# Kernel tuning notes

Measured on AMD Instinct MI355X. Metric: run time of the kernel, lower is better.

## Reference

```python
import jax, jax.numpy as jnp
import numpy as np

GENE_NUM = 3000
N_NODES = 50000
N_EDGES = 1000000
DIM = 128


def setup_inputs() -> dict:
    key = jax.random.key(0)
    ks = jax.random.split(key, 8)
    h = jax.random.normal(ks[0], (N_NODES, DIM), dtype=jnp.float32)
    alpha = jax.random.normal(ks[1], (GENE_NUM + 2,), dtype=jnp.float32)
    edge_weight = jax.random.uniform(ks[2], (N_EDGES,), dtype=jnp.float32)
    # Xavier-uniform Linear weight, zero bias
    gain = float(np.sqrt(2.0))  # calculate_gain('relu')
    bound = gain * np.sqrt(6.0 / (DIM + DIM))
    W = jax.random.uniform(ks[3], (DIM, DIM), minval=-bound, maxval=bound, dtype=jnp.float32)
    b = jnp.zeros((DIM,), dtype=jnp.float32)
    # node ids: genes 0..GENE_NUM-1 have id = gene index (>=0); cells have id = -1 (<0)
    node_id = jnp.concatenate([
        jnp.arange(GENE_NUM, dtype=jnp.int64),
        -jnp.ones((N_NODES - GENE_NUM,), dtype=jnp.int64),
    ])
    edge_src = jax.random.randint(ks[4], (N_EDGES,), 0, N_NODES, dtype=jnp.int64)
    edge_dst = jax.random.randint(ks[5], (N_EDGES,), 0, N_NODES, dtype=jnp.int64)
    return {"h": h, "alpha": alpha, "edge_weight": edge_weight, "W": W, "b": b,
            "node_id": node_id, "edge_src": edge_src, "edge_dst": edge_dst}


def reference(h, alpha, edge_weight, W, b, node_id, edge_src, edge_dst):
    gene_num = alpha.shape[0] - 2
    src_id = node_id[edge_src]  # [E]
    dst_id = node_id[edge_dst]  # [E]
    # default: cell self-loop alpha -> index gene_num + 1
    idx = jnp.full(edge_src.shape, gene_num + 1, dtype=jnp.int32)
    idx = jnp.where((src_id >= 0) & (dst_id < 0), src_id.astype(jnp.int32), idx)   # gene->cell: beta[src]
    idx = jnp.where((dst_id >= 0) & (src_id < 0), dst_id.astype(jnp.int32), idx)   # cell->gene: beta[dst]
    idx = jnp.where((dst_id >= 0) & (src_id >= 0), gene_num, idx)                  # gene self-loop alpha
    # gather -> per-edge message [E, D]
    coeff = alpha[idx] * edge_weight                     # [E]
    msg = h[edge_src] * coeff[:, None]                   # [E, D]
    # scatter-mean over destination nodes
    n = h.shape[0]
    summ = jax.ops.segment_sum(msg, edge_dst, num_segments=n)           # [N, D]
    cnt = jax.ops.segment_sum(jnp.ones_like(edge_weight), edge_dst, num_segments=n)
    neigh = summ / jnp.maximum(cnt, 1.0)[:, None]
    # MLP: dropout(eval, identity) -> Linear -> ReLU -> norm(identity)
    z = jax.nn.relu(neigh @ W.T + b)
    return z
```

## Files before the change

kernel.cpp:

```cpp
#include <hip/hip_runtime.h>

#define D 128
#define PSHIFT 6
#define PSIZE 64
#define EDGES_PER_BLK 4096
#define CAP 2048
#define MAXPART 1024
#define NCHUNK 4

typedef __attribute__((ext_vector_type(8))) short bf16x8;
typedef __attribute__((ext_vector_type(4))) float f32x4;

__device__ __forceinline__ unsigned short f2bf(float f) {
  unsigned int u = __float_as_uint(f);
  u = (u + 0x7fffu + ((u >> 16) & 1)) >> 16;
  return (unsigned short)u;
}

__global__ __launch_bounds__(512) void cvt_hist_kernel(
    const float* __restrict__ h, unsigned short* __restrict__ h16, int total4,
    const int* __restrict__ edst, int* __restrict__ g_hist, int E,
    int cvtBlocks, int N) {
  if ((int)blockIdx.x < cvtBlocks) {
    int i = blockIdx.x * 512 + threadIdx.x;
    if (i >= total4) return;
    float4 v = ((const float4*)h)[i];
    ushort4 o;
    o.x = f2bf(v.x); o.y = f2bf(v.y); o.z = f2bf(v.z); o.w = f2bf(v.w);
    int f = i * 4;
    int n = f >> 7;
    int d = f & 127;
    int c = d >> 5;
    int wi = d & 31;
    ((ushort4*)h16)[(size_t)c * N * 8 + n * 8 + (wi >> 2)] = o;
    return;
  }
  __shared__ int cnt[MAXPART];
  int t = threadIdx.x;
  cnt[t] = 0; cnt[t + 512] = 0;
  __syncthreads();
  int eb = (blockIdx.x - cvtBlocks) * EDGES_PER_BLK;
#pragma unroll
  for (int q = 0; q < 8; ++q) {
    int e = eb + q * 512 + t;
    if (e < E) atomicAdd(&cnt[edst[e] >> PSHIFT], 1);
  }
  __syncthreads();
  int c = cnt[t];
  if (c > 0) atomicAdd(&g_hist[t], c);
  c = cnt[t + 512];
  if (c > 0) atomicAdd(&g_hist[t + 512], c);
}

__global__ __launch_bounds__(512) void part_scan_kernel(
    const int* __restrict__ g_hist, int* __restrict__ part_off,
    int* __restrict__ g_cursor, int E, int npart) {
  __shared__ int ts[512];
  int t = threadIdx.x;
  int i0 = 2 * t, i1 = 2 * t + 1;
  int v0 = (i0 < npart) ? g_hist[i0] : 0;
  int v1 = (i1 < npart) ? g_hist[i1] : 0;
  ts[t] = v0 + v1;
  __syncthreads();
  for (int off = 1; off < 512; off <<= 1) {
    int x = (t >= off) ? ts[t - off] : 0;
    __syncthreads();
    ts[t] += x;
    __syncthreads();
  }
  int excl = ts[t] - (v0 + v1);
  if (i0 < npart) { part_off[i0] = excl; g_cursor[i0] = excl; }
  if (i1 < npart) { part_off[i1] = excl + v0; g_cursor[i1] = excl + v0; }
  if (t == 0) part_off[npart] = E;
}

__global__ __launch_bounds__(512) void bin_scatter_kernel(
    const float* __restrict__ alpha, const float* __restrict__ ew,
    const int* __restrict__ node_id, const int* __restrict__ esrc,
    const int* __restrict__ edst, int* __restrict__ g_cursor,
    int2* __restrict__ recs, int E, int gene_num) {
  __shared__ int2 lrec[EDGES_PER_BLK];
  __shared__ unsigned short lbin[EDGES_PER_BLK];
  __shared__ int cnt[MAXPART], offl[MAXPART], gbase[MAXPART];
  __shared__ int ts[512];

  int t = threadIdx.x;
  cnt[t] = 0; cnt[t + 512] = 0;
  __syncthreads();

  int eb = blockIdx.x * EDGES_PER_BLK;
  int rx[8]; float rc[8]; int rb[8]; int rk[8];
#pragma unroll
  for (int q = 0; q < 8; ++q) {
    int e = eb + q * 512 + t;
    rk[q] = -1;
    if (e < E) {
      int src = esrc[e];
      int dst = edst[e];
      int sid = node_id[src];
      int did = node_id[dst];
      int idx;
      if (sid >= 0) idx = (did >= 0) ? gene_num : sid;
      else          idx = (did >= 0) ? did : (gene_num + 1);
      rc[q] = alpha[idx] * ew[e];
      rx[q] = src | ((dst & (PSIZE - 1)) << 16);
      int b = dst >> PSHIFT;
      rb[q] = b;
      rk[q] = atomicAdd(&cnt[b], 1);
    }
  }
  __syncthreads();

  int c0 = cnt[2 * t], c1 = cnt[2 * t + 1];
  ts[t] = c0 + c1;
  __syncthreads();
  for (int off = 1; off < 512; off <<= 1) {
    int x = (t >= off) ? ts[t - off] : 0;
    __syncthreads();
    ts[t] += x;
    __syncthreads();
  }
  int exclp = ts[t] - (c0 + c1);
  offl[2 * t] = exclp;
  offl[2 * t + 1] = exclp + c0;
  __syncthreads();

#pragma unroll
  for (int q = 0; q < 8; ++q) {
    if (rk[q] >= 0) {
      int ls = offl[rb[q]] + rk[q];
      lrec[ls] = make_int2(rx[q], __float_as_int(rc[q]));
      lbin[ls] = (unsigned short)rb[q];
    }
  }
  __syncthreads();

  {
    int c = cnt[t];
    if (c > 0) gbase[t] = atomicAdd(&g_cursor[t], c);
    c = cnt[t + 512];
    if (c > 0) gbase[t + 512] = atomicAdd(&g_cursor[t + 512], c);
  }
  __syncthreads();

  int tot = E - eb;
  if (tot > EDGES_PER_BLK) tot = EDGES_PER_BLK;
  for (int s = t; s < tot; s += 512) {
    int b = lbin[s];
    recs[gbase[b] + (s - offl[b])] = lrec[s];
  }
}

__global__ __launch_bounds__(512) void sort_kernel(
    int2* __restrict__ recs, const int* __restrict__ part_off,
    int* __restrict__ cnt_g, int* __restrict__ off_g,
    int* __restrict__ rk_g) {
  __shared__ int2 lrec[CAP];
  __shared__ int cnt[PSIZE], offl[PSIZE];

  int t = threadIdx.x;
  int p = blockIdx.x;
  if (t < PSIZE) cnt[t] = 0;
  __syncthreads();

  int start = part_off[p];
  int R = part_off[p + 1] - start;
  if (R > CAP) R = CAP;

  int2 rq[4]; int dlq[4]; int rkq[4];
#pragma unroll
  for (int q = 0; q < 4; ++q) {
    int s = q * 512 + t;
    rkq[q] = -1;
    if (s < R) {
      int2 r = recs[start + s];
      rq[q] = r;
      int dl = (r.x >> 16) & (PSIZE - 1);
      dlq[q] = dl;
      rkq[q] = atomicAdd(&cnt[dl], 1);
    }
  }
  __syncthreads();

  if (t < PSIZE) offl[t] = cnt[t];
  __syncthreads();
  for (int off = 1; off < PSIZE; off <<= 1) {
    int x = 0;
    if (t < PSIZE && t >= off) x = offl[t - off];
    __syncthreads();
    if (t < PSIZE) offl[t] += x;
    __syncthreads();
  }
  if (t < PSIZE) offl[t] -= cnt[t];
  __syncthreads();

#pragma unroll
  for (int q = 0; q < 4; ++q)
    if (rkq[q] >= 0) lrec[offl[dlq[q]] + rkq[q]] = rq[q];
  __syncthreads();

  for (int s = t; s < R; s += 512) recs[start + s] = lrec[s];
  if (t < PSIZE) {
    cnt_g[p * PSIZE + t] = cnt[t];
    off_g[p * PSIZE + t] = offl[t];
    int my = cnt[t];
    int r = 0;
    for (int j = 0; j < PSIZE; ++j) {
      int cj = cnt[j];
      r += (cj > my) || (cj == my && j < t);
    }
    rk_g[p * PSIZE + r] = t;
  }
}

__global__ __launch_bounds__(512) void part_acc_kernel(
    const unsigned short* __restrict__ h16, const int2* __restrict__ recs,
    const int* __restrict__ part_off, const int* __restrict__ cnt_g,
    const int* __restrict__ off_g, const int* __restrict__ rk_g,
    float* __restrict__ neigh, int N) {
  int t = threadIdx.x;
  int p = blockIdx.x >> 2;
  int chunk = blockIdx.x & 3;
  int start = part_off[p];

  int w = t >> 6;
  int l = t & 63;
  int esub = l >> 4;
  int dpair = l & 15;
  const unsigned int* hpc =
      ((const unsigned int*)h16) + (size_t)chunk * N * 16 + dpair;

#pragma unroll
  for (int h2 = 0; h2 < 2; ++h2) {
    int Q = (h2 == 0) ? w : (15 - w);
    int myDl = rk_g[p * PSIZE + Q * 4 + esub];
    int myCnt = cnt_g[p * PSIZE + myDl];
    int myBase = start + off_g[p * PSIZE + myDl];
    float ax = 0.f, ay = 0.f;
    int k = 0;
    for (; k + 8 <= myCnt; k += 8) {
      unsigned int v[8]; float c[8];
#pragma unroll
      for (int q = 0; q < 8; ++q) {
        int2 r = recs[myBase + k + q];
        c[q] = __int_as_float(r.y);
        v[q] = hpc[(size_t)(r.x & 0xffff) * 16];
      }
#pragma unroll
      for (int q = 0; q < 8; ++q) {
        ax += c[q] * __uint_as_float(v[q] << 16);
        ay += c[q] * __uint_as_float(v[q] & 0xffff0000u);
      }
    }
    for (; k < myCnt; k += 4) {
      unsigned int v[4]; float c[4];
#pragma unroll
      for (int q = 0; q < 4; ++q) {
        int sl = k + q;
        int2 r = recs[myBase + sl];
        bool ok = sl < myCnt;
        c[q] = ok ? __int_as_float(r.y) : 0.f;
        unsigned int a = ok ? (unsigned int)(r.x & 0xffff) : 0u;
        v[q] = hpc[(size_t)a * 16];
      }
#pragma unroll
      for (int q = 0; q < 4; ++q) {
        ax += c[q] * __uint_as_float(v[q] << 16);
        ay += c[q] * __uint_as_float(v[q] & 0xffff0000u);
      }
    }
    int dst = p * PSIZE + myDl;
    if (dst < N) {
      float inv = 1.0f / (float)(myCnt > 0 ? myCnt : 1);
      ((float2*)neigh)[(size_t)dst * 64 + chunk * 16 + dpair] =
          make_float2(ax * inv, ay * inv);
    }
  }
}

__global__ __launch_bounds__(256) void mlp_mfma_kernel(
    const float* __restrict__ W, const float* __restrict__ bias,
    float* __restrict__ io, int N) {
  __shared__ __align__(16) unsigned short Wl[128 * 128];

  int t = threadIdx.x;
#pragma unroll
  for (int i = 0; i < 8; ++i) {
    int chunk = t + 256 * i;
    int row = chunk >> 4;
    int cb = chunk & 15;
    const float* gp = W + (size_t)row * 128 + cb * 8;
    float4 a = *(const float4*)gp;
    float4 b = *(const float4*)(gp + 4);
    bf16x8 v;
    v[0] = (short)f2bf(a.x); v[1] = (short)f2bf(a.y);
    v[2] = (short)f2bf(a.z); v[3] = (short)f2bf(a.w);
    v[4] = (short)f2bf(b.x); v[5] = (short)f2bf(b.y);
    v[6] = (short)f2bf(b.z); v[7] = (short)f2bf(b.w);
    *(bf16x8*)((char*)Wl + row * 256 + ((cb ^ (row & 7)) << 4)) = v;
  }
  __syncthreads();

  int l = t & 63;
  int w = t >> 6;
  int kg = l >> 4;
  int m_base = blockIdx.x * 64 + w * 16;
  int arow = m_base + (l & 15);
  if (arow >= N) arow = N - 1;

  bf16x8 af[4];
  const float* ap = io + (size_t)arow * 128 + kg * 8;
#pragma unroll
  for (int kk = 0; kk < 4; ++kk) {
    float4 a = *(const float4*)(ap + kk * 32);
    float4 b = *(const float4*)(ap + kk * 32 + 4);
    bf16x8 v;
    v[0] = (short)f2bf(a.x); v[1] = (short)f2bf(a.y);
    v[2] = (short)f2bf(a.z); v[3] = (short)f2bf(a.w);
    v[4] = (short)f2bf(b.x); v[5] = (short)f2bf(b.y);
    v[6] = (short)f2bf(b.z); v[7] = (short)f2bf(b.w);
    af[kk] = v;
  }

#pragma unroll
  for (int c = 0; c < 8; ++c) {
    f32x4 acc = {0.f, 0.f, 0.f, 0.f};
    int row_w = c * 16 + (l & 15);
    int rs = row_w & 7;
#pragma unroll
    for (int kk = 0; kk < 4; ++kk) {
      int cb = kk * 4 + kg;
      bf16x8 bf = *(bf16x8*)((char*)Wl + row_w * 256 + ((cb ^ rs) << 4));
      acc = __builtin_amdgcn_mfma_f32_16x16x32_bf16(af[kk], bf, acc, 0, 0, 0);
    }
    int j = c * 16 + (l & 15);
    float bj = bias[j];
#pragma unroll
    for (int r = 0; r < 4; ++r) {
      int m = m_base + kg * 4 + r;
      if (m < N) io[(size_t)m * 128 + j] = fmaxf(acc[r] + bj, 0.0f);
    }
  }
}

extern "C" void kernel_launch(void* const* d_in, const int* in_sizes, int n_in,
                              void* d_out, int out_size, void* d_ws, size_t ws_size,
                              hipStream_t stream) {
  const float* h     = (const float*)d_in[0];
  const float* alpha = (const float*)d_in[1];
  const float* ew    = (const float*)d_in[2];
  const float* W     = (const float*)d_in[3];
  const float* bias  = (const float*)d_in[4];
  const int* node_id = (const int*)d_in[5];
  const int* esrc    = (const int*)d_in[6];
  const int* edst    = (const int*)d_in[7];
  float* out = (float*)d_out;

  int E = in_sizes[2];
  int N = in_sizes[5];
  int gene_num = in_sizes[1] - 2;
  int npart = (N + PSIZE - 1) / PSIZE;
  int eblocks = (E + EDGES_PER_BLK - 1) / EDGES_PER_BLK;
  int total4 = N * D / 4;
  int cvtBlocks = (total4 + 511) / 512;

  int* g_hist   = (int*)d_ws;
  int* part_off = g_hist + MAXPART;
  int* g_cursor = part_off + MAXPART + 1;
  int* cnt_g    = g_cursor + MAXPART;
  int* off_g    = cnt_g + MAXPART * PSIZE;
  int* rk_g     = off_g + MAXPART * PSIZE;
  size_t h16_off = ((size_t)(3 * MAXPART + 1 + 3 * MAXPART * PSIZE) * sizeof(int)
                    + 15) & ~(size_t)15;
  unsigned short* h16 = (unsigned short*)((char*)d_ws + h16_off);
  size_t rec_off = (h16_off + (size_t)N * D * sizeof(unsigned short) + 15) & ~(size_t)15;
  int2* recs = (int2*)((char*)d_ws + rec_off);
  size_t need = rec_off + (size_t)(E + 8) * sizeof(int2);
  if (ws_size < need) return;

  hipMemsetAsync(g_hist, 0, MAXPART * sizeof(int), stream);

  cvt_hist_kernel<<<cvtBlocks + eblocks, 512, 0, stream>>>(
      h, h16, total4, edst, g_hist, E, cvtBlocks, N);
  part_scan_kernel<<<1, 512, 0, stream>>>(g_hist, part_off, g_cursor, E, npart);
  bin_scatter_kernel<<<eblocks, 512, 0, stream>>>(alpha, ew, node_id, esrc,
                                                  edst, g_cursor, recs, E,
                                                  gene_num);
  sort_kernel<<<npart, 512, 0, stream>>>(recs, part_off, cnt_g, off_g, rk_g);
  part_acc_kernel<<<npart * NCHUNK, 512, 0, stream>>>(h16, recs, part_off,
                                                      cnt_g, off_g, rk_g,
                                                      out, N);
  {
    int blocks = (N + 63) / 64;
    mlp_mfma_kernel<<<blocks, 256, 0, stream>>>(W, bias, out, N);
  }
}
```

Measured before the change: 122.5 us.

## Pack edge records into 32-bit src+bf16 coeff and stage padded buckets in LDS

Edge records shrink from 8-byte int2 to a 4-byte word holding the source index and a bf16 coefficient, with the destination-local index kept in a separate byte array. The sort kernel writes each partition into a fixed-stride buffer whose per-destination buckets are padded to multiples of four with zero records. The accumulate kernel loads the partition's records into LDS once and reads them from there, without tail masking. The aim is to cut record traffic across the scatter, sort and accumulate kernels and avoid repeated global record reads across the four chunk blocks. In exchange the coefficient is rounded to bf16, and partitions larger than PSTRIDE would overflow; source indices must also fit in 16 bits.

New measurement: 109.1 us. 1.12x faster.

```diff
diff --git a/kernel.cpp b/kernel.cpp
--- a/kernel.cpp
+++ b/kernel.cpp
@@ -5,6 +5,7 @@
 #define PSIZE 64
 #define EDGES_PER_BLK 4096
 #define CAP 2048
+#define PSTRIDE 2240
 #define MAXPART 1024
 #define NCHUNK 4
 
@@ -78,9 +79,11 @@
     const float* __restrict__ alpha, const float* __restrict__ ew,
     const int* __restrict__ node_id, const int* __restrict__ esrc,
     const int* __restrict__ edst, int* __restrict__ g_cursor,
-    int2* __restrict__ recs, int E, int gene_num) {
-  __shared__ int2 lrec[EDGES_PER_BLK];
+    unsigned int* __restrict__ recs4, unsigned char* __restrict__ dl8,
+    int E, int gene_num) {
+  __shared__ unsigned int lrec[EDGES_PER_BLK];
   __shared__ unsigned short lbin[EDGES_PER_BLK];
+  __shared__ unsigned char ldl[EDGES_PER_BLK];
   __shared__ int cnt[MAXPART], offl[MAXPART], gbase[MAXPART];
   __shared__ int ts[512];
 
@@ -89,7 +92,7 @@
   __syncthreads();
 
   int eb = blockIdx.x * EDGES_PER_BLK;
-  int rx[8]; float rc[8]; int rb[8]; int rk[8];
+  unsigned int rx[8]; int rb[8]; int rk[8]; int rdl[8];
 #pragma unroll
   for (int q = 0; q < 8; ++q) {
     int e = eb + q * 512 + t;
@@ -102,8 +105,9 @@
       int idx;
       if (sid >= 0) idx = (did >= 0) ? gene_num : sid;
       else          idx = (did >= 0) ? did : (gene_num + 1);
-      rc[q] = alpha[idx] * ew[e];
-      rx[q] = src | ((dst & (PSIZE - 1)) << 16);
+      float coeff = alpha[idx] * ew[e];
+      rx[q] = (unsigned int)src | ((unsigned int)f2bf(coeff) << 16);
+      rdl[q] = dst & (PSIZE - 1);
       int b = dst >> PSHIFT;
       rb[q] = b;
       rk[q] = atomicAdd(&cnt[b], 1);
@@ -129,8 +133,9 @@
   for (int q = 0; q < 8; ++q) {
     if (rk[q] >= 0) {
       int ls = offl[rb[q]] + rk[q];
-      lrec[ls] = make_int2(rx[q], __float_as_int(rc[q]));
+      lrec[ls] = rx[q];
       lbin[ls] = (unsigned short)rb[q];
+      ldl[ls] = (unsigned char)rdl[q];
     }
   }
   __syncthreads();
@@ -147,62 +152,66 @@
   if (tot > EDGES_PER_BLK) tot = EDGES_PER_BLK;
   for (int s = t; s < tot; s += 512) {
     int b = lbin[s];
-    recs[gbase[b] + (s - offl[b])] = lrec[s];
+    int pos = gbase[b] + (s - offl[b]);
+    recs4[pos] = lrec[s];
+    dl8[pos] = ldl[s];
   }
 }
 
 __global__ __launch_bounds__(512) void sort_kernel(
-    int2* __restrict__ recs, const int* __restrict__ part_off,
-    int* __restrict__ cnt_g, int* __restrict__ off_g,
-    int* __restrict__ rk_g) {
-  __shared__ int2 lrec[CAP];
-  __shared__ int cnt[PSIZE], offl[PSIZE];
+    const unsigned int* __restrict__ recs4, const unsigned char* __restrict__ dl8,
+    const int* __restrict__ part_off, unsigned int* __restrict__ recs4p,
+    int* __restrict__ cnt_g, int* __restrict__ pad_g, int* __restrict__ rk_g) {
+  __shared__ unsigned int lrec[PSTRIDE];
+  __shared__ int cnt[PSIZE], padl[PSIZE];
 
   int t = threadIdx.x;
   int p = blockIdx.x;
   if (t < PSIZE) cnt[t] = 0;
+  for (int s = t; s < PSTRIDE; s += 512) lrec[s] = 0u;
   __syncthreads();
 
   int start = part_off[p];
   int R = part_off[p + 1] - start;
   if (R > CAP) R = CAP;
 
-  int2 rq[4]; int dlq[4]; int rkq[4];
+  unsigned int rq[4]; int dlq[4]; int rkq[4];
 #pragma unroll
   for (int q = 0; q < 4; ++q) {
     int s = q * 512 + t;
     rkq[q] = -1;
     if (s < R) {
-      int2 r = recs[start + s];
-      rq[q] = r;
-      int dl = (r.x >> 16) & (PSIZE - 1);
+      rq[q] = recs4[start + s];
+      int dl = dl8[start + s];
       dlq[q] = dl;
       rkq[q] = atomicAdd(&cnt[dl], 1);
     }
   }
   __syncthreads();
 
-  if (t < PSIZE) offl[t] = cnt[t];
+  if (t < PSIZE) padl[t] = (cnt[t] + 3) & ~3;
   __syncthreads();
   for (int off = 1; off < PSIZE; off <<= 1) {
     int x = 0;
-    if (t < PSIZE && t >= off) x = offl[t - off];
-    __syncthreads();
-    if (t < PSIZE) offl[t] += x;
-    __syncthreads();
-  }
-  if (t < PSIZE) offl[t] -= cnt[t];
+    if (t < PSIZE && t >= off) x = padl[t - off];
+    __syncthreads();
+    if (t < PSIZE) padl[t] += x;
+    __syncthreads();
+  }
+  if (t < PSIZE) padl[t] -= (cnt[t] + 3) & ~3;
   __syncthreads();
 
 #pragma unroll
   for (int q = 0; q < 4; ++q)
-    if (rkq[q] >= 0) lrec[offl[dlq[q]] + rkq[q]] = rq[q];
-  __syncthreads();
-
-  for (int s = t; s < R; s += 512) recs[start + s] = lrec[s];
+    if (rkq[q] >= 0) lrec[padl[dlq[q]] + rkq[q]] = rq[q];
+  __syncthreads();
+
+  int padTot = padl[PSIZE - 1] + ((cnt[PSIZE - 1] + 3) & ~3);
+  for (int s = t; s < padTot; s += 512)
+    recs4p[(size_t)p * PSTRIDE + s] = lrec[s];
   if (t < PSIZE) {
     cnt_g[p * PSIZE + t] = cnt[t];
-    off_g[p * PSIZE + t] = offl[t];
+    pad_g[p * PSIZE + t] = padl[t];
     int my = cnt[t];
     int r = 0;
     for (int j = 0; j < PSIZE; ++j) {
@@ -214,14 +223,20 @@
 }
 
 __global__ __launch_bounds__(512) void part_acc_kernel(
-    const unsigned short* __restrict__ h16, const int2* __restrict__ recs,
-    const int* __restrict__ part_off, const int* __restrict__ cnt_g,
-    const int* __restrict__ off_g, const int* __restrict__ rk_g,
-    float* __restrict__ neigh, int N) {
+    const unsigned short* __restrict__ h16, const unsigned int* __restrict__ recs4p,
+    const int* __restrict__ cnt_g, const int* __restrict__ pad_g,
+    const int* __restrict__ rk_g, float* __restrict__ neigh, int N) {
+  __shared__ unsigned int lrec[PSTRIDE];
+
   int t = threadIdx.x;
   int p = blockIdx.x >> 2;
   int chunk = blockIdx.x & 3;
-  int start = part_off[p];
+
+  int padTot = pad_g[p * PSIZE + PSIZE - 1] +
+               ((cnt_g[p * PSIZE + PSIZE - 1] + 3) & ~3);
+  for (int s = t; s < padTot; s += 512)
+    lrec[s] = recs4p[(size_t)p * PSTRIDE + s];
+  __syncthreads();
 
   int w = t >> 6;
   int l = t & 63;
@@ -235,16 +250,17 @@
     int Q = (h2 == 0) ? w : (15 - w);
     int myDl = rk_g[p * PSIZE + Q * 4 + esub];
     int myCnt = cnt_g[p * PSIZE + myDl];
-    int myBase = start + off_g[p * PSIZE + myDl];
+    int myOff = pad_g[p * PSIZE + myDl];
+    int myPad = (myCnt + 3) & ~3;
     float ax = 0.f, ay = 0.f;
     int k = 0;
-    for (; k + 8 <= myCnt; k += 8) {
+    for (; k + 8 <= myPad; k += 8) {
       unsigned int v[8]; float c[8];
 #pragma unroll
       for (int q = 0; q < 8; ++q) {
-        int2 r = recs[myBase + k + q];
-        c[q] = __int_as_float(r.y);
-        v[q] = hpc[(size_t)(r.x & 0xffff) * 16];
+        unsigned int r = lrec[myOff + k + q];
+        c[q] = __uint_as_float(r & 0xffff0000u);
+        v[q] = hpc[(size_t)(r & 0xffffu) * 16];
       }
 #pragma unroll
       for (int q = 0; q < 8; ++q) {
@@ -252,16 +268,13 @@
         ay += c[q] * __uint_as_float(v[q] & 0xffff0000u);
       }
     }
-    for (; k < myCnt; k += 4) {
+    if (k < myPad) {
       unsigned int v[4]; float c[4];
 #pragma unroll
       for (int q = 0; q < 4; ++q) {
-        int sl = k + q;
-        int2 r = recs[myBase + sl];
-        bool ok = sl < myCnt;
-        c[q] = ok ? __int_as_float(r.y) : 0.f;
-        unsigned int a = ok ? (unsigned int)(r.x & 0xffff) : 0u;
-        v[q] = hpc[(size_t)a * 16];
+        unsigned int r = lrec[myOff + k + q];
+        c[q] = __uint_as_float(r & 0xffff0000u);
+        v[q] = hpc[(size_t)(r & 0xffffu) * 16];
       }
 #pragma unroll
       for (int q = 0; q < 4; ++q) {
@@ -368,14 +381,18 @@
   int* part_off = g_hist + MAXPART;
   int* g_cursor = part_off + MAXPART + 1;
   int* cnt_g    = g_cursor + MAXPART;
-  int* off_g    = cnt_g + MAXPART * PSIZE;
-  int* rk_g     = off_g + MAXPART * PSIZE;
+  int* pad_g    = cnt_g + MAXPART * PSIZE;
+  int* rk_g     = pad_g + MAXPART * PSIZE;
   size_t h16_off = ((size_t)(3 * MAXPART + 1 + 3 * MAXPART * PSIZE) * sizeof(int)
                     + 15) & ~(size_t)15;
   unsigned short* h16 = (unsigned short*)((char*)d_ws + h16_off);
-  size_t rec_off = (h16_off + (size_t)N * D * sizeof(unsigned short) + 15) & ~(size_t)15;
-  int2* recs = (int2*)((char*)d_ws + rec_off);
-  size_t need = rec_off + (size_t)(E + 8) * sizeof(int2);
+  size_t r4_off = (h16_off + (size_t)N * D * sizeof(unsigned short) + 15) & ~(size_t)15;
+  unsigned int* recs4 = (unsigned int*)((char*)d_ws + r4_off);
+  size_t dl_off = (r4_off + (size_t)(E + 8) * 4 + 15) & ~(size_t)15;
+  unsigned char* dl8 = (unsigned char*)((char*)d_ws + dl_off);
+  size_t r4p_off = (dl_off + (size_t)(E + 8) + 15) & ~(size_t)15;
+  unsigned int* recs4p = (unsigned int*)((char*)d_ws + r4p_off);
+  size_t need = r4p_off + (size_t)npart * PSTRIDE * 4;
   if (ws_size < need) return;
 
   hipMemsetAsync(g_hist, 0, MAXPART * sizeof(int), stream);
@@ -384,12 +401,12 @@
       h, h16, total4, edst, g_hist, E, cvtBlocks, N);
   part_scan_kernel<<<1, 512, 0, stream>>>(g_hist, part_off, g_cursor, E, npart);
   bin_scatter_kernel<<<eblocks, 512, 0, stream>>>(alpha, ew, node_id, esrc,
-                                                  edst, g_cursor, recs, E,
-                                                  gene_num);
-  sort_kernel<<<npart, 512, 0, stream>>>(recs, part_off, cnt_g, off_g, rk_g);
-  part_acc_kernel<<<npart * NCHUNK, 512, 0, stream>>>(h16, recs, part_off,
-                                                      cnt_g, off_g, rk_g,
-                                                      out, N);
+                                                  edst, g_cursor, recs4, dl8,
+                                                  E, gene_num);
+  sort_kernel<<<npart, 512, 0, stream>>>(recs4, dl8, part_off, recs4p,
+                                         cnt_g, pad_g, rk_g);
+  part_acc_kernel<<<npart * NCHUNK, 512, 0, stream>>>(h16, recs4p, cnt_g,
+                                                      pad_g, rk_g, out, N);
   {
     int blocks = (N + 63) / 64;
     mlp_mfma_kernel<<<blocks, 256, 0, stream>>>(W, bias, out, N);
```
